# Kernel tuning notes

Hardware: AMD Instinct MI355X
Metric: run time of the kernel (lower is better)

## Reference

```python
import jax, jax.numpy as jnp
import numpy as np

N_NODES = 50000


def gcn_conv(x, edge_index, W, b):
    # PyG GCNConv: h = X @ W; add self-loops; sym-normalize; scatter-add to target; + bias
    N = x.shape[0]
    h = x @ W
    src = jnp.concatenate([edge_index[0], jnp.arange(N)])
    dst = jnp.concatenate([edge_index[1], jnp.arange(N)])
    ew = jnp.ones(src.shape[0], dtype=h.dtype)
    deg = jax.ops.segment_sum(ew, dst, num_segments=N)
    dinv = jnp.where(deg > 0, deg ** -0.5, 0.0)
    norm = dinv[src] * ew * dinv[dst]              # [E+N]
    msg = h[src] * norm[:, None]                   # gather + scale
    out = jax.ops.segment_sum(msg, dst, num_segments=N)  # scatter-add
    return out + b


def setup_inputs() -> dict:
    key = jax.random.key(0)
    ks = jax.random.split(key, 8)
    x = jax.random.normal(ks[0], (N_NODES, 128), dtype=jnp.float32)
    edge_index = jax.random.randint(ks[1], (2, 800000), 0, N_NODES)
    W1 = jax.random.normal(ks[2], (128, 96), dtype=jnp.float32) * 0.1
    b1 = jax.random.normal(ks[3], (96,), dtype=jnp.float32) * 0.1
    W_mu = jax.random.normal(ks[4], (96, 64), dtype=jnp.float32) * 0.1
    b_mu = jax.random.normal(ks[5], (64,), dtype=jnp.float32) * 0.1
    W_lv = jax.random.normal(ks[6], (96, 64), dtype=jnp.float32) * 0.1
    b_lv = jax.random.normal(ks[7], (64,), dtype=jnp.float32) * 0.1
    return {"x": x, "edge_index": edge_index, "W1": W1, "b1": b1,
            "W_mu": W_mu, "b_mu": b_mu, "W_lv": W_lv, "b_lv": b_lv}


def reference(x, edge_index, W1, b1, W_mu, b_mu, W_lv, b_lv):
    h = jax.nn.relu(gcn_conv(x, edge_index, W1, b1))
    mu = gcn_conv(h, edge_index, W_mu, b_mu).sum(axis=0, keepdims=True)      # SumAggregation -> [1, out]
    logvar = gcn_conv(h, edge_index, W_lv, b_lv).sum(axis=0, keepdims=True)  # [1, out]
    return (mu, logvar)
```

## Files before the change

### kernel.cpp

```cpp
#include <hip/hip_runtime.h>
#include <hip/hip_fp16.h>


#define NCHUNK 32
#define LOG_NCHUNK 5
#define NSLICE 16
#define SLICE_MAX 3136
#define SORT_T 1024

typedef float v2f __attribute__((ext_vector_type(2)));
typedef float f32x4 __attribute__((ext_vector_type(4)));
typedef _Float16 half8 __attribute__((ext_vector_type(8)));

__device__ inline unsigned f2h(float a, float b) {
    __half2 h = __floats2half2_rn(a, b);
    return *reinterpret_cast<unsigned*>(&h);
}

__device__ inline unsigned pk_fp8(float a, float b, float c, float d) {
    int p = __builtin_amdgcn_cvt_pk_fp8_f32(a, b, 0, false);
    p = __builtin_amdgcn_cvt_pk_fp8_f32(c, d, p, true);
    return (unsigned)p;
}

__device__ inline void add_fp8(float4& acc, unsigned u) {
    v2f f;
    f = __builtin_amdgcn_cvt_pk_f32_fp8(u, false); acc.x += f.x; acc.y += f.y;
    f = __builtin_amdgcn_cvt_pk_f32_fp8(u, true);  acc.z += f.x; acc.w += f.y;
}

__launch_bounds__(SORT_T)
__global__ void k_count(const int* __restrict__ dst, unsigned short* __restrict__ pcount,
                        int N, int E, int chunkE, int sliceN) {
    int c = blockIdx.x & (NCHUNK - 1), s = blockIdx.x >> LOG_NCHUNK;
    int nbase = s * sliceN;
    __shared__ int hist[SLICE_MAX];
    for (int j = threadIdx.x; j < sliceN; j += SORT_T) hist[j] = 0;
    __syncthreads();
    int e0 = c * chunkE, e1 = min(e0 + chunkE, E);
    int ne = e1 - e0;
    const int4* d4 = (const int4*)(dst + e0);
    int n4 = ne >> 2;
    for (int i = threadIdx.x; i < n4; i += SORT_T) {
        int4 d = d4[i];
        unsigned q;
        q = (unsigned)(d.x - nbase); if (q < (unsigned)sliceN) atomicAdd(&hist[q], 1);
        q = (unsigned)(d.y - nbase); if (q < (unsigned)sliceN) atomicAdd(&hist[q], 1);
        q = (unsigned)(d.z - nbase); if (q < (unsigned)sliceN) atomicAdd(&hist[q], 1);
        q = (unsigned)(d.w - nbase); if (q < (unsigned)sliceN) atomicAdd(&hist[q], 1);
    }
    if (threadIdx.x < (ne & 3)) {
        int d = dst[e0 + (n4 << 2) + threadIdx.x];
        unsigned q = (unsigned)(d - nbase);
        if (q < (unsigned)sliceN) atomicAdd(&hist[q], 1);
    }
    __syncthreads();
    for (int j = threadIdx.x; j < sliceN; j += SORT_T) {
        int n = nbase + j;
        if (n < N) pcount[(size_t)c * N + n] = (unsigned short)hist[j];
    }
}

__launch_bounds__(256)
__global__ void k_degdinv(const unsigned short* __restrict__ pcount, int* __restrict__ deg,
                          float* __restrict__ dinv, int* __restrict__ blocksum, int N) {
    int tid = threadIdx.x;
    int n = blockIdx.x * 256 + tid;
    int s = 0;
    if (n < N) {
        #pragma unroll
        for (int c = 0; c < NCHUNK; ++c) s += pcount[(size_t)c * N + n];
        deg[n] = s;
        dinv[n] = rsqrtf((float)(s + 1));
    }
    __shared__ int sh[256];
    sh[tid] = s;
    __syncthreads();
    #pragma unroll
    for (int off = 128; off; off >>= 1) {
        if (tid < off) sh[tid] += sh[tid + off];
        __syncthreads();
    }
    if (tid == 0) blocksum[blockIdx.x] = sh[0];
}

__launch_bounds__(256)
__global__ void k_offs(const unsigned short* __restrict__ pcount, int* __restrict__ offs,
                       const int* __restrict__ deg, const int* __restrict__ blocksum,
                       int* __restrict__ rowptr, int N, int E, int nb) {
    int tid = threadIdx.x;
    __shared__ int sh[256];
    int bs = (tid < nb && tid < (int)blockIdx.x) ? blocksum[tid] : 0;
    sh[tid] = bs;
    __syncthreads();
    #pragma unroll
    for (int off = 128; off; off >>= 1) {
        if (tid < off) sh[tid] += sh[tid + off];
        __syncthreads();
    }
    int blockoff = sh[0];
    __syncthreads();
    int n = blockIdx.x * 256 + tid;
    int v = (n < N) ? deg[n] : 0;
    sh[tid] = v;
    __syncthreads();
    for (int off = 1; off < 256; off <<= 1) {
        int t = (tid >= off) ? sh[tid - off] : 0;
        __syncthreads();
        sh[tid] += t;
        __syncthreads();
    }
    int run = blockoff + sh[tid] - v;
    if (n < N) {
        rowptr[n] = run;
        #pragma unroll
        for (int c = 0; c < NCHUNK; ++c) {
            size_t ix = (size_t)c * N + n;
            int t = pcount[ix];
            offs[ix] = run;
            run += t;
        }
    }
    if (blockIdx.x == 0 && tid == 0) rowptr[N] = E;
}

__launch_bounds__(SORT_T)
__global__ void k_place(const int* __restrict__ src, const int* __restrict__ dst,
                        const float* __restrict__ dinv, int* __restrict__ offs,
                        int* __restrict__ col, int N, int E, int chunkE, int sliceN) {
    int c = blockIdx.x & (NCHUNK - 1), s = blockIdx.x >> LOG_NCHUNK;
    int nbase = s * sliceN;
    __shared__ int cur[SLICE_MAX];
    __shared__ float rs[SLICE_MAX];
    for (int j = threadIdx.x; j < sliceN; j += SORT_T) {
        int n = nbase + j;
        cur[j] = (n < N) ? offs[(size_t)c * N + n] : 0;
        rs[j] = 0.f;
    }
    __syncthreads();
    int e0 = c * chunkE, e1 = min(e0 + chunkE, E);
    int ne = e1 - e0;
    const int4* s4 = (const int4*)(src + e0);
    const int4* d4 = (const int4*)(dst + e0);
    int n4 = ne >> 2;
    for (int i = threadIdx.x; i < n4; i += SORT_T) {
        int4 sv = s4[i];
        int4 dv = d4[i];
        unsigned qd, qs;
        qd = (unsigned)(dv.x - nbase);
        if (qd < (unsigned)sliceN) { int p = atomicAdd(&cur[qd], 1); col[p] = sv.x; }
        qs = (unsigned)(sv.x - nbase);
        if (qs < (unsigned)sliceN) atomicAdd(&rs[qs], dinv[dv.x]);
        qd = (unsigned)(dv.y - nbase);
        if (qd < (unsigned)sliceN) { int p = atomicAdd(&cur[qd], 1); col[p] = sv.y; }
        qs = (unsigned)(sv.y - nbase);
        if (qs < (unsigned)sliceN) atomicAdd(&rs[qs], dinv[dv.y]);
        qd = (unsigned)(dv.z - nbase);
        if (qd < (unsigned)sliceN) { int p = atomicAdd(&cur[qd], 1); col[p] = sv.z; }
        qs = (unsigned)(sv.z - nbase);
        if (qs < (unsigned)sliceN) atomicAdd(&rs[qs], dinv[dv.z]);
        qd = (unsigned)(dv.w - nbase);
        if (qd < (unsigned)sliceN) { int p = atomicAdd(&cur[qd], 1); col[p] = sv.w; }
        qs = (unsigned)(sv.w - nbase);
        if (qs < (unsigned)sliceN) atomicAdd(&rs[qs], dinv[dv.w]);
    }
    if (threadIdx.x < (ne & 3)) {
        int e = e0 + (n4 << 2) + threadIdx.x;
        int sv = src[e], dv = dst[e];
        unsigned qd = (unsigned)(dv - nbase);
        if (qd < (unsigned)sliceN) { int p = atomicAdd(&cur[qd], 1); col[p] = sv; }
        unsigned qs = (unsigned)(sv - nbase);
        if (qs < (unsigned)sliceN) atomicAdd(&rs[qs], dinv[dv]);
    }
    __syncthreads();
    float* prs = (float*)offs;
    for (int j = threadIdx.x; j < sliceN; j += SORT_T) {
        int n = nbase + j;
        if (n < N) prs[(size_t)c * N + n] = rs[j];
    }
}

__launch_bounds__(256)
__global__ void k_gemm(const float* __restrict__ x, const float* __restrict__ W1,
                       const float* __restrict__ dinv, const float* __restrict__ prs,
                       float* __restrict__ cfac, unsigned* __restrict__ g, int n) {
    __shared__ float Ws[128 * 96];
    __shared__ uint4 Whu4[24 * 64];
    int tid = threadIdx.x;
    {
        const float4* wsrc = (const float4*)W1;
        float4* wdst = (float4*)Ws;
        #pragma unroll
        for (int i = 0; i < 12; ++i) wdst[tid + 256 * i] = wsrc[tid + 256 * i];
    }
    {
        int r = blockIdx.x * 64 + tid;
        if (tid < 64 && r < n) {
            float s = 0.f;
            #pragma unroll
            for (int c = 0; c < NCHUNK; ++c) s += prs[(size_t)c * n + r];
            float dv = dinv[r];
            cfac[r] = dv * (dv + s);
        }
    }
    __syncthreads();

    for (int idx = tid; idx < 24 * 64; idx += 256) {
        int lane = idx & 63;
        int frag = idx >> 6;
        int ks = frag / 6, ct = frag - ks * 6;
        int k0 = ks * 32 + (lane >> 4) * 8;
        int c = ct * 16 + (lane & 15);
        const float* wsp = Ws + (size_t)k0 * 96 + c;
        Whu4[idx] = make_uint4(f2h(wsp[0],   wsp[96]),
                               f2h(wsp[192], wsp[288]),
                               f2h(wsp[384], wsp[480]),
                               f2h(wsp[576], wsp[672]));
    }
    __syncthreads();

    int wid = tid >> 6, lane = tid & 63;
    int xrow = blockIdx.x * 64 + wid * 16 + (lane & 15);
    bool vrow = xrow < n;
    const float4* xp = (const float4*)(x + (size_t)(vrow ? xrow : 0) * 128);

    f32x4 acc[6];
    #pragma unroll
    for (int ct = 0; ct < 6; ++ct) acc[ct] = (f32x4){0.f, 0.f, 0.f, 0.f};

    #pragma unroll
    for (int ks = 0; ks < 4; ++ks) {
        float4 xa = xp[ks * 8 + (lane >> 4) * 2];
        float4 xb = xp[ks * 8 + (lane >> 4) * 2 + 1];
        half8 bf;
        bf[0] = (_Float16)xa.x; bf[1] = (_Float16)xa.y;
        bf[2] = (_Float16)xa.z; bf[3] = (_Float16)xa.w;
        bf[4] = (_Float16)xb.x; bf[5] = (_Float16)xb.y;
        bf[6] = (_Float16)xb.z; bf[7] = (_Float16)xb.w;
        #pragma unroll
        for (int ct = 0; ct < 6; ++ct) {
            half8 af = *reinterpret_cast<const half8*>(&Whu4[(ks * 6 + ct) * 64 + lane]);
            acc[ct] = __builtin_amdgcn_mfma_f32_16x16x32_f16(af, bf, acc[ct], 0, 0, 0);
        }
    }

    if (vrow) {
        float dv = dinv[xrow] * 16.f;
        unsigned* o = g + (size_t)xrow * 24 + (lane >> 4);
        #pragma unroll
        for (int ct = 0; ct < 6; ++ct) {
            o[ct * 4] = pk_fp8(acc[ct][0] * dv, acc[ct][1] * dv,
                               acc[ct][2] * dv, acc[ct][3] * dv);
        }
    }
}

#define AGG_NODES 16
#define AGG_T (AGG_NODES * 24)
__launch_bounds__(AGG_T)
__global__ void k_agg(const unsigned* __restrict__ g1, const int* __restrict__ col,
                      const int* __restrict__ rowptr, const float* __restrict__ dinv,
                      const float* __restrict__ cfac, const float* __restrict__ b1,
                      float* __restrict__ v_part, int n) {
    int tid = threadIdx.x;
    int nl = tid / 24;
    int ch = tid % 24;
    int d = blockIdx.x * AGG_NODES + nl;

    __shared__ float4 sh[AGG_NODES][24];

    float4 contrib = make_float4(0.f, 0.f, 0.f, 0.f);
    if (d < n) {
        float dds = dinv[d] * 0.0625f;
        int e0 = rowptr[d], e1 = rowptr[d + 1];
        float4 aA = make_float4(0.f, 0.f, 0.f, 0.f);
        float4 aB = make_float4(0.f, 0.f, 0.f, 0.f);
        float4 aC = make_float4(0.f, 0.f, 0.f, 0.f);
        float4 aD = make_float4(0.f, 0.f, 0.f, 0.f);
        int e = e0;
        for (; e + 8 <= e1; e += 8) {
            int s0 = __builtin_nontemporal_load(col + e);
            int s1 = __builtin_nontemporal_load(col + e + 1);
            int s2 = __builtin_nontemporal_load(col + e + 2);
            int s3 = __builtin_nontemporal_load(col + e + 3);
            int s4 = __builtin_nontemporal_load(col + e + 4);
            int s5 = __builtin_nontemporal_load(col + e + 5);
            int s6 = __builtin_nontemporal_load(col + e + 6);
            int s7 = __builtin_nontemporal_load(col + e + 7);
            unsigned u0 = g1[(size_t)s0 * 24 + ch];
            unsigned u1 = g1[(size_t)s1 * 24 + ch];
            unsigned u2 = g1[(size_t)s2 * 24 + ch];
            unsigned u3 = g1[(size_t)s3 * 24 + ch];
            unsigned u4 = g1[(size_t)s4 * 24 + ch];
            unsigned u5 = g1[(size_t)s5 * 24 + ch];
            unsigned u6 = g1[(size_t)s6 * 24 + ch];
            unsigned u7 = g1[(size_t)s7 * 24 + ch];
            add_fp8(aA, u0); add_fp8(aB, u1); add_fp8(aC, u2); add_fp8(aD, u3);
            add_fp8(aA, u4); add_fp8(aB, u5); add_fp8(aC, u6); add_fp8(aD, u7);
        }
        for (; e + 2 <= e1; e += 2) {
            int s0 = __builtin_nontemporal_load(col + e);
            int s1 = __builtin_nontemporal_load(col + e + 1);
            unsigned u0 = g1[(size_t)s0 * 24 + ch];
            unsigned u1 = g1[(size_t)s1 * 24 + ch];
            add_fp8(aA, u0); add_fp8(aB, u1);
        }
        if (e < e1) {
            int s0 = __builtin_nontemporal_load(col + e);
            add_fp8(aC, g1[(size_t)s0 * 24 + ch]);
        }
        add_fp8(aD, g1[(size_t)d * 24 + ch]);
        float4 b1c = ((const float4*)b1)[ch];
        float cd = cfac[d];
        float hx = fmaxf(fmaf(dds, (aA.x + aB.x) + (aC.x + aD.x), b1c.x), 0.f);
        float hy = fmaxf(fmaf(dds, (aA.y + aB.y) + (aC.y + aD.y), b1c.y), 0.f);
        float hz = fmaxf(fmaf(dds, (aA.z + aB.z) + (aC.z + aD.z), b1c.z), 0.f);
        float hw = fmaxf(fmaf(dds, (aA.w + aB.w) + (aC.w + aD.w), b1c.w), 0.f);
        contrib = make_float4(cd * hx, cd * hy, cd * hz, cd * hw);
    }
    sh[nl][ch] = contrib;
    __syncthreads();
    #pragma unroll
    for (int off = 8; off >= 1; off >>= 1) {
        if (nl < off) {
            float4 a = sh[nl][ch];
            float4 b = sh[nl + off][ch];
            a.x += b.x; a.y += b.y; a.z += b.z; a.w += b.w;
            sh[nl][ch] = a;
        }
        __syncthreads();
    }
    if (tid < 24) {
        ((float4*)(v_part + (size_t)blockIdx.x * 96))[tid] = sh[0][tid];
    }
}

__global__ void k_vred(const float* __restrict__ vp, float* __restrict__ v, int nb) {
    int j = blockIdx.x;
    float s = 0.f;
    for (int i = threadIdx.x; i < nb; i += 256) s += vp[(size_t)i * 96 + j];
    __shared__ float sh[256];
    sh[threadIdx.x] = s;
    __syncthreads();
    for (int off = 128; off; off >>= 1) {
        if (threadIdx.x < off) sh[threadIdx.x] += sh[threadIdx.x + off];
        __syncthreads();
    }
    if (threadIdx.x == 0) v[j] = sh[0];
}

__global__ void k_out(const float* __restrict__ v,
                      const float* __restrict__ Wmu, const float* __restrict__ bmu,
                      const float* __restrict__ Wlv, const float* __restrict__ blv,
                      float* __restrict__ out, float nN) {
    int tid = threadIdx.x;
    const float* W = (tid < 64) ? Wmu : Wlv;
    const float* b = (tid < 64) ? bmu : blv;
    int j = tid & 63;
    float s = 0.f;
    #pragma unroll
    for (int k = 0; k < 96; ++k) s = fmaf(v[k], W[k * 64 + j], s);
    out[tid] = s + nN * b[j];
}

extern "C" void kernel_launch(void* const* d_in, const int* in_sizes, int n_in,
                              void* d_out, int out_size, void* d_ws, size_t ws_size,
                              hipStream_t stream) {
    const float* x   = (const float*)d_in[0];
    const int*   ei  = (const int*)d_in[1];
    const float* W1  = (const float*)d_in[2];
    const float* b1  = (const float*)d_in[3];
    const float* Wmu = (const float*)d_in[4];
    const float* bmu = (const float*)d_in[5];
    const float* Wlv = (const float*)d_in[6];
    const float* blv = (const float*)d_in[7];
    float* out = (float*)d_out;

    const int N = in_sizes[0] / 128;
    const int E = in_sizes[1] / 2;
    const int* src = ei;
    const int* dst = ei + E;

    const int chunkE = (((E + NCHUNK - 1) / NCHUNK) + 3) & ~3;
    const int sliceN = (N + NSLICE - 1) / NSLICE;
    const int gN = (N + 255) / 256;

    size_t off = 0;
    auto alloc = [&](size_t bytes) -> char* {
        off = (off + 255) & ~(size_t)255;
        char* p = (char*)d_ws + off;
        off += bytes;
        return p;
    };
    unsigned short* pcount = (unsigned short*)alloc((size_t)NCHUNK * N * 2);
    int*      offsb    = (int*)alloc((size_t)NCHUNK * N * 4);
    int*      rowptr   = (int*)alloc((size_t)(N + 1) * 4);
    int*      col      = (int*)alloc((size_t)E * 4);
    int*      deg      = (int*)alloc((size_t)N * 4);
    float*    dinv     = (float*)alloc((size_t)N * 4);
    float*    cfac     = (float*)alloc((size_t)N * 4);
    int*      blocksum = (int*)alloc((size_t)gN * 4);
    unsigned* g        = (unsigned*)alloc((size_t)N * 96);
    const int nAggBlocks = (N + AGG_NODES - 1) / AGG_NODES;
    float*    v_part   = (float*)alloc((size_t)nAggBlocks * 96 * 4);
    float*    v        = (float*)alloc(96 * 4);

    k_count<<<NCHUNK * NSLICE, SORT_T, 0, stream>>>(dst, pcount, N, E, chunkE, sliceN);
    k_degdinv<<<gN, 256, 0, stream>>>(pcount, deg, dinv, blocksum, N);
    k_offs<<<gN, 256, 0, stream>>>(pcount, offsb, deg, blocksum, rowptr, N, E, gN);
    k_place<<<NCHUNK * NSLICE, SORT_T, 0, stream>>>(src, dst, dinv, offsb, col, N, E, chunkE, sliceN);
    k_gemm<<<(N + 63) / 64, 256, 0, stream>>>(x, W1, dinv, (const float*)offsb, cfac, g, N);
    k_agg<<<nAggBlocks, AGG_T, 0, stream>>>(g, col, rowptr, dinv, cfac, b1, v_part, N);
    k_vred<<<96, 256, 0, stream>>>(v_part, v, nAggBlocks);
    k_out<<<1, 128, 0, stream>>>(v, Wmu, bmu, Wlv, blv, out, (float)N);
}
```

Baseline: 83.67 us.

## Halve edge chunk count and fuse final reduction with output projection

Cuts the number of edge chunks used in the counting sort from 32 to 16, which halves the per-chunk count and offset arrays and the blocks in count/place. It also removes the last launch by initializing the output with the scaled bias inside the degree kernel and having each reduction block atomically add its projected contribution. This trades one kernel launch and a round-trip through global memory for 96x128 float atomics on the output, and fewer, larger chunks may raise per-block work and histogram contention.

```diff
diff --git a/kernel.cpp b/kernel.cpp
--- a/kernel.cpp
+++ b/kernel.cpp
@@ -2,8 +2,8 @@
 #include <hip/hip_fp16.h>
 
 
-#define NCHUNK 32
-#define LOG_NCHUNK 5
+#define NCHUNK 16
+#define LOG_NCHUNK 4
 #define NSLICE 16
 #define SLICE_MAX 3136
 #define SORT_T 1024
@@ -63,8 +63,13 @@
 
 __launch_bounds__(256)
 __global__ void k_degdinv(const unsigned short* __restrict__ pcount, int* __restrict__ deg,
-                          float* __restrict__ dinv, int* __restrict__ blocksum, int N) {
+                          float* __restrict__ dinv, int* __restrict__ blocksum,
+                          const float* __restrict__ bmu, const float* __restrict__ blv,
+                          float* __restrict__ out, float nN, int N) {
     int tid = threadIdx.x;
+    if (blockIdx.x == 0 && tid < 128) {
+        out[tid] = nN * ((tid < 64) ? bmu[tid] : blv[tid - 64]);
+    }
     int n = blockIdx.x * 256 + tid;
     int s = 0;
     if (n < N) {
@@ -335,32 +340,27 @@
     }
 }
 
-__global__ void k_vred(const float* __restrict__ vp, float* __restrict__ v, int nb) {
+__launch_bounds__(256)
+__global__ void k_vredout(const float* __restrict__ vp, int nb,
+                          const float* __restrict__ Wmu, const float* __restrict__ Wlv,
+                          float* __restrict__ out) {
     int j = blockIdx.x;
+    int tid = threadIdx.x;
     float s = 0.f;
-    for (int i = threadIdx.x; i < nb; i += 256) s += vp[(size_t)i * 96 + j];
+    for (int i = tid; i < nb; i += 256) s += vp[(size_t)i * 96 + j];
     __shared__ float sh[256];
-    sh[threadIdx.x] = s;
+    sh[tid] = s;
     __syncthreads();
     for (int off = 128; off; off >>= 1) {
-        if (threadIdx.x < off) sh[threadIdx.x] += sh[threadIdx.x + off];
-        __syncthreads();
-    }
-    if (threadIdx.x == 0) v[j] = sh[0];
-}
-
-__global__ void k_out(const float* __restrict__ v,
-                      const float* __restrict__ Wmu, const float* __restrict__ bmu,
-                      const float* __restrict__ Wlv, const float* __restrict__ blv,
-                      float* __restrict__ out, float nN) {
-    int tid = threadIdx.x;
-    const float* W = (tid < 64) ? Wmu : Wlv;
-    const float* b = (tid < 64) ? bmu : blv;
-    int j = tid & 63;
-    float s = 0.f;
-    #pragma unroll
-    for (int k = 0; k < 96; ++k) s = fmaf(v[k], W[k * 64 + j], s);
-    out[tid] = s + nN * b[j];
+        if (tid < off) sh[tid] += sh[tid + off];
+        __syncthreads();
+    }
+    float vj = sh[0];
+    if (tid < 128) {
+        const float* W = (tid < 64) ? Wmu : Wlv;
+        int jj = tid & 63;
+        atomicAdd(&out[tid], vj * W[(size_t)j * 64 + jj]);
+    }
 }
 
 extern "C" void kernel_launch(void* const* d_in, const int* in_sizes, int n_in,
@@ -403,14 +403,12 @@
     unsigned* g        = (unsigned*)alloc((size_t)N * 96);
     const int nAggBlocks = (N + AGG_NODES - 1) / AGG_NODES;
     float*    v_part   = (float*)alloc((size_t)nAggBlocks * 96 * 4);
-    float*    v        = (float*)alloc(96 * 4);
 
     k_count<<<NCHUNK * NSLICE, SORT_T, 0, stream>>>(dst, pcount, N, E, chunkE, sliceN);
-    k_degdinv<<<gN, 256, 0, stream>>>(pcount, deg, dinv, blocksum, N);
+    k_degdinv<<<gN, 256, 0, stream>>>(pcount, deg, dinv, blocksum, bmu, blv, out, (float)N, N);
     k_offs<<<gN, 256, 0, stream>>>(pcount, offsb, deg, blocksum, rowptr, N, E, gN);
     k_place<<<NCHUNK * NSLICE, SORT_T, 0, stream>>>(src, dst, dinv, offsb, col, N, E, chunkE, sliceN);
     k_gemm<<<(N + 63) / 64, 256, 0, stream>>>(x, W1, dinv, (const float*)offsb, cfac, g, N);
     k_agg<<<nAggBlocks, AGG_T, 0, stream>>>(g, col, rowptr, dinv, cfac, b1, v_part, N);
-    k_vred<<<96, 256, 0, stream>>>(v_part, v, nAggBlocks);
-    k_out<<<1, 128, 0, stream>>>(v, Wmu, bmu, Wlv, blv, out, (float)N);
-}
+    k_vredout<<<96, 256, 0, stream>>>(v_part, nAggBlocks, Wmu, Wlv, out);
+}
```

Measured after the change: 89.37 us. +6.8%, slower.
